# Performance work log

Hardware: AMD Instinct MI355X
Metric: run time of the kernel (lower is better)

## Reference

```python
import jax, jax.numpy as jnp
from jax import lax
import numpy as np

H = 64  # hidden_size


def _gru_layer(x, w_ih, w_hh, b_ih, b_hh):
    """Single GRU layer, batch_first. x: [B, T, Din] -> [B, T, H].
    PyTorch gate order: r, z, n.
    """
    B = x.shape[0]
    # Precompute input projections for all timesteps: [B, T, 3H] -> [T, B, 3H]
    gi = jnp.einsum('bti,gi->btg', x, w_ih) + b_ih
    gi = jnp.moveaxis(gi, 1, 0)

    def step(h, g):
        gh = h @ w_hh.T + b_hh                      # [B, 3H]
        i_r, i_z, i_n = jnp.split(g, 3, axis=-1)
        h_r, h_z, h_n = jnp.split(gh, 3, axis=-1)
        r = jax.nn.sigmoid(i_r + h_r)
        z = jax.nn.sigmoid(i_z + h_z)
        n = jnp.tanh(i_n + r * h_n)
        h_new = (1.0 - z) * n + z * h
        return h_new, h_new

    h0 = jnp.zeros((B, w_hh.shape[1]), x.dtype)
    _, ys = lax.scan(step, h0, gi)                  # ys: [T, B, H]
    return jnp.moveaxis(ys, 0, 1)                   # [B, T, H]


def setup_inputs() -> dict:
    key = jax.random.key(0)
    ks = jax.random.split(key, 12)
    B, T = 4096, 512
    s = 1.0 / np.sqrt(H)  # PyTorch GRU init scale
    u = lambda k, shp: jax.random.uniform(k, shp, jnp.float32, -s, s)
    return {
        'x': jax.random.normal(ks[0], (B, T, 1), jnp.float32),
        # layer 0: input_size=1
        'w_ih0': u(ks[1], (3 * H, 1)),
        'w_hh0': u(ks[2], (3 * H, H)),
        'b_ih0': u(ks[3], (3 * H,)),
        'b_hh0': u(ks[4], (3 * H,)),
        # layer 1: input_size=H
        'w_ih1': u(ks[5], (3 * H, H)),
        'w_hh1': u(ks[6], (3 * H, H)),
        'b_ih1': u(ks[7], (3 * H,)),
        'b_hh1': u(ks[8], (3 * H,)),
        # final linear head H -> 1
        'fc_w': u(ks[9], (1, H)),
        'fc_b': u(ks[10], (1,)),
    }


def reference(x, w_ih0, w_hh0, b_ih0, b_hh0, w_ih1, w_hh1, b_ih1, b_hh1, fc_w, fc_b):
    h1 = _gru_layer(x, w_ih0, w_hh0, b_ih0, b_hh0)   # [B, T, H]
    h2 = _gru_layer(h1, w_ih1, w_hh1, b_ih1, b_hh1)  # [B, T, H]
    last = h2[:, -1, :]                              # [B, H]
    return last @ fc_w.T + fc_b                      # [B, 1]
```

## Files before the change

### kernel.cpp

```cpp
#include <hip/hip_runtime.h>


typedef _Float16 half8 __attribute__((ext_vector_type(8)));
typedef float    v4f   __attribute__((ext_vector_type(4)));
typedef float    v2f   __attribute__((ext_vector_type(2)));
typedef unsigned uint4v __attribute__((ext_vector_type(4)));

#define T_LEN 512
#define KS 72

#define L2E  1.4426950408889634f
#define L2E2 2.8853900817779268f

static __device__ __forceinline__ v4f mfma16(half8 a, half8 b, v4f c) {
    return __builtin_amdgcn_mfma_f32_16x16x32_f16(a, b, c, 0, 0, 0);
}
static __device__ __forceinline__ half8 ld8(const _Float16* p) {
    return *(const half8*)p;
}
static __device__ __forceinline__ v2f exp2v(v2f x) {
    v2f r; r.x = __builtin_amdgcn_exp2f(x.x); r.y = __builtin_amdgcn_exp2f(x.y);
    return r;
}
static __device__ __forceinline__ v2f rcpv(v2f x) {
    v2f r; r.x = __builtin_amdgcn_rcpf(x.x); r.y = __builtin_amdgcn_rcpf(x.y);
    return r;
}
static __device__ __forceinline__ void gru_cell4(
        v2f arA, v2f arB, v2f azA, v2f azB,
        v2f niA, v2f niB, v2f nhA, v2f nhB,
        v2f hA,  v2f hB,  v2f* oA, v2f* oB) {
    const v2f CA = exp2v(arA);
    const v2f CB = exp2v(arB);
    const v2f AA = exp2v(azA);
    const v2f AB = exp2v(azB);
    const v2f rA = rcpv(CA + 1.0f);
    const v2f rB = rcpv(CB + 1.0f);
    const v2f wnA = __builtin_elementwise_fma(rA, nhA, niA);
    const v2f wnB = __builtin_elementwise_fma(rB, nhB, niB);
    const v2f BvA = exp2v(wnA);
    const v2f BvB = exp2v(wnB);
    const v2f aBA = BvA + 1.0f;
    const v2f aBB = BvB + 1.0f;
    const v2f numA = __builtin_elementwise_fma(hA, aBA, AA * (1.0f - BvA));
    const v2f numB = __builtin_elementwise_fma(hB, aBB, AB * (1.0f - BvB));
    const v2f denA = (AA + 1.0f) * aBA;
    const v2f denB = (AB + 1.0f) * aBB;
    *oA = numA * rcpv(denA);
    *oB = numB * rcpv(denB);
}

__global__ __launch_bounds__(512, 1)
void gru_mfma(const float* __restrict__ x,
              const float* __restrict__ w_ih0, const float* __restrict__ w_hh0,
              const float* __restrict__ b_ih0, const float* __restrict__ b_hh0,
              const float* __restrict__ w_ih1, const float* __restrict__ w_hh1,
              const float* __restrict__ b_ih1, const float* __restrict__ b_hh1,
              const float* __restrict__ fc_w,  const float* __restrict__ fc_b,
              float* __restrict__ out)
{
    __shared__ __align__(16) unsigned xh32[T_LEN * 16];
    __shared__ __align__(16) _Float16 h0f[2][16 * KS];
    __shared__ __align__(16) _Float16 h1f[2][16 * KS];
    __shared__ float red[64];

    const int tid  = threadIdx.x;
    const int wv   = tid >> 6;
    const int grp  = wv >> 2;
    const int w    = wv & 3;
    const int lane = tid & 63;
    const int n    = lane & 15;
    const int q    = lane >> 4;
    const int u    = w * 16 + n;

    const float* xg = x + (size_t)(blockIdx.x * 16) * T_LEN;
    for (int i = tid; i < 16 * T_LEN; i += 512) {
        const int row = i >> 9, t = i & 511;
        const float v = xg[row * T_LEN + t];
        xh32[t * 16 + row] =
            (unsigned)__builtin_bit_cast(unsigned short, (_Float16)v);
    }
    for (int i = tid; i < 16 * KS; i += 512) {
        h0f[1][i] = (_Float16)0;
        h1f[1][i] = (_Float16)0;
    }

    half8 B[3][4];
    {
        const int rows[3] = {u, 64 + u, 128 + u};
        const float sc[3] = {-L2E, -L2E, -L2E2};
        const float* bc[4];
        if (grp == 0) {
            bc[0] = w_hh0;      bc[1] = w_hh0 + 32;
            bc[2] = w_hh0;      bc[3] = w_hh0 + 32;
        } else {
            bc[0] = w_ih1;      bc[1] = w_ih1 + 32;
            bc[2] = w_hh1;      bc[3] = w_hh1 + 32;
        }
        #pragma unroll
        for (int g = 0; g < 3; g++)
            #pragma unroll
            for (int c = 0; c < 4; c++) {
                const float* r0 = bc[c] + rows[g] * 64 + 8 * q;
                #pragma unroll
                for (int j = 0; j < 8; j++) B[g][c][j] = (_Float16)(r0[j] * sc[g]);
            }
    }

    half8 BX[3];
    {
        const float sc3[3] = {-L2E, -L2E, -L2E2};
        #pragma unroll
        for (int g = 0; g < 3; g++) {
            uint4v z = {0u, 0u, 0u, 0u};
            if (grp == 0 && q == 0) {
                const _Float16 wv16 = (_Float16)(w_ih0[g * 64 + u] * sc3[g]);
                z.x = (unsigned)__builtin_bit_cast(unsigned short, wv16);
            }
            BX[g] = __builtin_bit_cast(half8, z);
        }
    }

    float brc, bzc, binc, bhnc;
    if (grp == 0) {
        brc = -(b_ih0[u] + b_hh0[u]) * L2E;
        bzc = -(b_ih0[64 + u] + b_hh0[64 + u]) * L2E;
        binc = -b_ih0[128 + u] * L2E2; bhnc = -b_hh0[128 + u] * L2E2;
    } else {
        brc = -(b_ih1[u] + b_hh1[u]) * L2E;
        bzc = -(b_ih1[64 + u] + b_hh1[64 + u]) * L2E;
        binc = -b_ih1[128 + u] * L2E2; bhnc = -b_hh1[128 + u] * L2E2;
    }

    const v4f biasR4  = {brc,  brc,  brc,  brc};
    const v4f biasZ4  = {bzc,  bzc,  bzc,  bzc};
    const v4f biasNi4 = {binc, binc, binc, binc};
    const v4f biasNh4 = {bhnc, bhnc, bhnc, bhnc};
    const v4f zero4   = {0.f, 0.f, 0.f, 0.f};

    v2f hA = {0.f, 0.f}, hB = {0.f, 0.f};

    __syncthreads();

    const int abase = n * KS + 8 * q;

    unsigned xwcur = (grp == 0) ? xh32[n] : 0u;

    auto grp0_step = [&](int k, int P) __attribute__((always_inline)) {
        const int pw = P, pr = P ^ 1;
        const half8 a0 = ld8(&h0f[pr][abase]);
        const half8 a1 = ld8(&h0f[pr][abase + 32]);
        uint4v ax32 = {0u, 0u, 0u, 0u};
        ax32.x = (q == 0) ? xwcur : 0u;
        const half8 ax = __builtin_bit_cast(half8, ax32);

        __builtin_amdgcn_s_setprio(1);
        v4f accR = mfma16(ax, BX[0], biasR4);
        v4f accZ = mfma16(ax, BX[1], biasZ4);
        v4f aNi  = mfma16(ax, BX[2], biasNi4);
        v4f accN = mfma16(a0, B[2][0], biasNh4);
        accR = mfma16(a0, B[0][0], accR);
        accZ = mfma16(a0, B[1][0], accZ);
        accN = mfma16(a1, B[2][1], accN);
        accR = mfma16(a1, B[0][1], accR);
        accZ = mfma16(a1, B[1][1], accZ);
        __builtin_amdgcn_s_setprio(0);

        xwcur = xh32[((k + 1) & (T_LEN - 1)) * 16 + n];

        v2f h01, h23;
        gru_cell4((v2f){accR[0], accR[1]}, (v2f){accR[2], accR[3]},
                  (v2f){accZ[0], accZ[1]}, (v2f){accZ[2], accZ[3]},
                  (v2f){aNi[0],  aNi[1]},  (v2f){aNi[2],  aNi[3]},
                  (v2f){accN[0], accN[1]}, (v2f){accN[2], accN[3]},
                  hA, hB, &h01, &h23);
        hA = h01; hB = h23;
        _Float16* wp = &h0f[pw][(4 * q) * KS + u];
        wp[0]      = (_Float16)h01.x;
        wp[KS]     = (_Float16)h01.y;
        wp[2 * KS] = (_Float16)h23.x;
        wp[3 * KS] = (_Float16)h23.y;
    };

    auto grp1_step = [&](int P) __attribute__((always_inline)) {
        const int pw = P ^ 1, p1 = P;
        const half8 g10 = ld8(&h1f[p1][abase]);
        const half8 g11 = ld8(&h1f[p1][abase + 32]);
        const half8 g00 = ld8(&h0f[pw][abase]);
        const half8 g01 = ld8(&h0f[pw][abase + 32]);

        __builtin_amdgcn_s_setprio(1);
        v4f aR1 = mfma16(g10, B[0][2], biasR4);
        v4f aZ1 = mfma16(g10, B[1][2], biasZ4);
        v4f aNh = mfma16(g10, B[2][2], biasNh4);
        aR1 = mfma16(g11, B[0][3], aR1);
        aZ1 = mfma16(g11, B[1][3], aZ1);
        aNh = mfma16(g11, B[2][3], aNh);
        v4f aR0 = mfma16(g00, B[0][0], zero4);
        v4f aZ0 = mfma16(g00, B[1][0], zero4);
        v4f aNi = mfma16(g00, B[2][0], biasNi4);
        aR0 = mfma16(g01, B[0][1], aR0);
        aZ0 = mfma16(g01, B[1][1], aZ0);
        aNi = mfma16(g01, B[2][1], aNi);
        __builtin_amdgcn_s_setprio(0);
        const v4f aR = aR1 + aR0;
        const v4f aZ = aZ1 + aZ0;

        v2f h01, h23;
        gru_cell4((v2f){aR[0], aR[1]},  (v2f){aR[2], aR[3]},
                  (v2f){aZ[0], aZ[1]},  (v2f){aZ[2], aZ[3]},
                  (v2f){aNi[0], aNi[1]}, (v2f){aNi[2], aNi[3]},
                  (v2f){aNh[0], aNh[1]}, (v2f){aNh[2], aNh[3]},
                  hA, hB, &h01, &h23);
        hA = h01; hB = h23;
        _Float16* wp = &h1f[pw][(4 * q) * KS + u];
        wp[0]      = (_Float16)h01.x;
        wp[KS]     = (_Float16)h01.y;
        wp[2 * KS] = (_Float16)h23.x;
        wp[3 * KS] = (_Float16)h23.y;
    };

    if (grp == 0) grp0_step(0, 0);
    __syncthreads();
    #pragma unroll 1
    for (int kk = 1; kk + 1 < T_LEN; kk += 2) {
        if (grp == 0) grp0_step(kk, 1); else grp1_step(1);
        __syncthreads();
        if (grp == 0) grp0_step(kk + 1, 0); else grp1_step(0);
        __syncthreads();
    }
    if (grp == 0) grp0_step(T_LEN - 1, 1); else grp1_step(1);
    __syncthreads();
    if (grp == 1) grp1_step(0);
    __syncthreads();

    if (grp == 1) {
        const float fw = fc_w[u];
        const float hv[4] = {hA.x, hA.y, hB.x, hB.y};
        #pragma unroll
        for (int r = 0; r < 4; r++) {
            float v = fw * hv[r];
            v += __shfl_xor(v, 1, 64);
            v += __shfl_xor(v, 2, 64);
            v += __shfl_xor(v, 4, 64);
            v += __shfl_xor(v, 8, 64);
            if (n == 0) red[(4 * q + r) * 4 + w] = v;
        }
    }
    __syncthreads();
    if (tid < 16) {
        const float s = red[tid * 4] + red[tid * 4 + 1] + red[tid * 4 + 2] + red[tid * 4 + 3];
        out[blockIdx.x * 16 + tid] = s + fc_b[0];
    }
}

extern "C" void kernel_launch(void* const* d_in, const int* in_sizes, int n_in,
                              void* d_out, int out_size, void* d_ws, size_t ws_size,
                              hipStream_t stream)
{
    const float* x     = (const float*)d_in[0];
    const float* w_ih0 = (const float*)d_in[1];
    const float* w_hh0 = (const float*)d_in[2];
    const float* b_ih0 = (const float*)d_in[3];
    const float* b_hh0 = (const float*)d_in[4];
    const float* w_ih1 = (const float*)d_in[5];
    const float* w_hh1 = (const float*)d_in[6];
    const float* b_ih1 = (const float*)d_in[7];
    const float* b_hh1 = (const float*)d_in[8];
    const float* fc_w  = (const float*)d_in[9];
    const float* fc_b  = (const float*)d_in[10];
    float* out = (float*)d_out;

    hipLaunchKernelGGL(gru_mfma, dim3(256), dim3(512), 0, stream,
                       x, w_ih0, w_hh0, b_ih0, b_hh0,
                       w_ih1, w_hh1, b_ih1, b_hh1, fc_w, fc_b, out);
}
```

Baseline: 314.4 us.

## Deepen layer-0 hidden ring buffer and prefetch layer-1 inputs one step ahead

The layer-0 hidden-state buffer grows from two to four slots so layer 1 can run one more step behind layer 0. Layer 1 now loads its layer-0 input into registers one phase early, which takes that LDS read off the critical path after each barrier. The MFMAs on the prefetched operand are reordered to issue first. The cost is more LDS, extra registers and one more pipeline phase at the end.

```diff
diff --git a/kernel.cpp b/kernel.cpp
--- a/kernel.cpp
+++ b/kernel.cpp
@@ -60,7 +60,7 @@
               float* __restrict__ out)
 {
     __shared__ __align__(16) unsigned xh32[T_LEN * 16];
-    __shared__ __align__(16) _Float16 h0f[2][16 * KS];
+    __shared__ __align__(16) _Float16 h0f[4][16 * KS];
     __shared__ __align__(16) _Float16 h1f[2][16 * KS];
     __shared__ float red[64];
 
@@ -81,7 +81,7 @@
             (unsigned)__builtin_bit_cast(unsigned short, (_Float16)v);
     }
     for (int i = tid; i < 16 * KS; i += 512) {
-        h0f[1][i] = (_Float16)0;
+        h0f[3][i] = (_Float16)0;
         h1f[1][i] = (_Float16)0;
     }
 
@@ -145,11 +145,13 @@
     const int abase = n * KS + 8 * q;
 
     unsigned xwcur = (grp == 0) ? xh32[n] : 0u;
-
-    auto grp0_step = [&](int k, int P) __attribute__((always_inline)) {
-        const int pw = P, pr = P ^ 1;
-        const half8 a0 = ld8(&h0f[pr][abase]);
-        const half8 a1 = ld8(&h0f[pr][abase + 32]);
+    half8 pf0 = {}, pf1 = {};
+
+    auto grp0_step = [&](int k, int PH) __attribute__((always_inline)) {
+        const _Float16* rp = &h0f[(PH + 3) & 3][0];
+        _Float16* wpb = &h0f[PH][0];
+        const half8 a0 = ld8(rp + abase);
+        const half8 a1 = ld8(rp + abase + 32);
         uint4v ax32 = {0u, 0u, 0u, 0u};
         ax32.x = (q == 0) ? xwcur : 0u;
         const half8 ax = __builtin_bit_cast(half8, ax32);
@@ -175,33 +177,40 @@
                   (v2f){accN[0], accN[1]}, (v2f){accN[2], accN[3]},
                   hA, hB, &h01, &h23);
         hA = h01; hB = h23;
-        _Float16* wp = &h0f[pw][(4 * q) * KS + u];
+        _Float16* wp = wpb + (4 * q) * KS + u;
         wp[0]      = (_Float16)h01.x;
         wp[KS]     = (_Float16)h01.y;
         wp[2 * KS] = (_Float16)h23.x;
         wp[3 * KS] = (_Float16)h23.y;
     };
 
-    auto grp1_step = [&](int P) __attribute__((always_inline)) {
-        const int pw = P ^ 1, p1 = P;
-        const half8 g10 = ld8(&h1f[p1][abase]);
-        const half8 g11 = ld8(&h1f[p1][abase + 32]);
-        const half8 g00 = ld8(&h0f[pw][abase]);
-        const half8 g01 = ld8(&h0f[pw][abase + 32]);
+    auto grp1_pf = [&](int PH) __attribute__((always_inline)) {
+        const _Float16* pp = &h0f[(PH + 3) & 3][0];
+        pf0 = ld8(pp + abase);
+        pf1 = ld8(pp + abase + 32);
+    };
+
+    auto grp1_step = [&](int PH, bool dopf) __attribute__((always_inline)) {
+        const int p1r = (PH & 1) ^ 1;
+        const int p1w = PH & 1;
+        const half8 g10 = ld8(&h1f[p1r][abase]);
+        const half8 g11 = ld8(&h1f[p1r][abase + 32]);
+        const half8 g00 = pf0, g01 = pf1;
+        if (dopf) grp1_pf(PH);
 
         __builtin_amdgcn_s_setprio(1);
+        v4f aR0 = mfma16(g00, B[0][0], zero4);
+        v4f aZ0 = mfma16(g00, B[1][0], zero4);
+        v4f aNi = mfma16(g00, B[2][0], biasNi4);
+        aR0 = mfma16(g01, B[0][1], aR0);
+        aZ0 = mfma16(g01, B[1][1], aZ0);
+        aNi = mfma16(g01, B[2][1], aNi);
         v4f aR1 = mfma16(g10, B[0][2], biasR4);
         v4f aZ1 = mfma16(g10, B[1][2], biasZ4);
         v4f aNh = mfma16(g10, B[2][2], biasNh4);
         aR1 = mfma16(g11, B[0][3], aR1);
         aZ1 = mfma16(g11, B[1][3], aZ1);
         aNh = mfma16(g11, B[2][3], aNh);
-        v4f aR0 = mfma16(g00, B[0][0], zero4);
-        v4f aZ0 = mfma16(g00, B[1][0], zero4);
-        v4f aNi = mfma16(g00, B[2][0], biasNi4);
-        aR0 = mfma16(g01, B[0][1], aR0);
-        aZ0 = mfma16(g01, B[1][1], aZ0);
-        aNi = mfma16(g01, B[2][1], aNi);
         __builtin_amdgcn_s_setprio(0);
         const v4f aR = aR1 + aR0;
         const v4f aZ = aZ1 + aZ0;
@@ -213,7 +222,7 @@
                   (v2f){aNh[0], aNh[1]}, (v2f){aNh[2], aNh[3]},
                   hA, hB, &h01, &h23);
         hA = h01; hB = h23;
-        _Float16* wp = &h1f[pw][(4 * q) * KS + u];
+        _Float16* wp = &h1f[p1w][(4 * q) * KS + u];
         wp[0]      = (_Float16)h01.x;
         wp[KS]     = (_Float16)h01.y;
         wp[2 * KS] = (_Float16)h23.x;
@@ -222,16 +231,26 @@
 
     if (grp == 0) grp0_step(0, 0);
     __syncthreads();
+    if (grp == 0) grp0_step(1, 1); else grp1_pf(1);
+    __syncthreads();
     #pragma unroll 1
-    for (int kk = 1; kk + 1 < T_LEN; kk += 2) {
-        if (grp == 0) grp0_step(kk, 1); else grp1_step(1);
-        __syncthreads();
-        if (grp == 0) grp0_step(kk + 1, 0); else grp1_step(0);
-        __syncthreads();
-    }
-    if (grp == 0) grp0_step(T_LEN - 1, 1); else grp1_step(1);
-    __syncthreads();
-    if (grp == 1) grp1_step(0);
+    for (int wb = 2; wb <= 506; wb += 4) {
+        if (grp == 0) grp0_step(wb,     2); else grp1_step(2, true);
+        __syncthreads();
+        if (grp == 0) grp0_step(wb + 1, 3); else grp1_step(3, true);
+        __syncthreads();
+        if (grp == 0) grp0_step(wb + 2, 0); else grp1_step(0, true);
+        __syncthreads();
+        if (grp == 0) grp0_step(wb + 3, 1); else grp1_step(1, true);
+        __syncthreads();
+    }
+    if (grp == 0) grp0_step(510, 2); else grp1_step(2, true);
+    __syncthreads();
+    if (grp == 0) grp0_step(511, 3); else grp1_step(3, true);
+    __syncthreads();
+    if (grp == 1) grp1_step(0, true);
+    __syncthreads();
+    if (grp == 1) grp1_step(1, false);
     __syncthreads();
 
     if (grp == 1) {
```

Measured after the change: 319.7 us. No clear change (+1.7%).
